# Kernel tuning notes

Hardware: AMD Instinct MI355X
Metric: run time of the kernel (lower is better)

## Reference

```python
import jax, jax.numpy as jnp
import numpy as np

EMBED_DIM = 512
NUM_HEADS = 8
WINDOW = 64
FFN_RATIO = 4


def _mha(q_in, kv_in, w_in, b_in, w_out, b_out, n_heads, mask=None):
    # Faithful torch.nn.MultiheadAttention (batch_first) with packed in_proj.
    b, sq, d = q_in.shape
    sk = kv_in.shape[1]
    hd = d // n_heads
    wq, wk, wv = jnp.split(w_in, 3, axis=0)   # each [d, d]
    bq, bk, bv = jnp.split(b_in, 3, axis=0)
    q = (q_in @ wq.T + bq).reshape(b, sq, n_heads, hd).transpose(0, 2, 1, 3)
    k = (kv_in @ wk.T + bk).reshape(b, sk, n_heads, hd).transpose(0, 2, 1, 3)
    v = (kv_in @ wv.T + bv).reshape(b, sk, n_heads, hd).transpose(0, 2, 1, 3)
    scores = jnp.einsum('bhqd,bhkd->bhqk', q, k) / jnp.sqrt(jnp.asarray(hd, q.dtype))
    if mask is not None:
        scores = scores + mask  # additive -inf mask, broadcast over [b, h]
    attn = jax.nn.softmax(scores, axis=-1)
    out = jnp.einsum('bhqk,bhkd->bhqd', attn, v)
    out = out.transpose(0, 2, 1, 3).reshape(b, sq, d)
    return out @ w_out.T + b_out


def _layernorm(x, g, b, eps=1e-5):
    mu = jnp.mean(x, axis=-1, keepdims=True)
    var = jnp.var(x, axis=-1, keepdims=True)
    return (x - mu) * jax.lax.rsqrt(var + eps) * g + b


def _local_causal_mask(p, window, dtype=jnp.float32):
    # row i attends to columns [max(0, i-window), i]
    i = jnp.arange(p)[:, None]
    j = jnp.arange(p)[None, :]
    allowed = (j <= i) & (j >= i - window)
    return jnp.where(allowed, jnp.zeros((), dtype), jnp.asarray(-jnp.inf, dtype))


def setup_inputs() -> dict:
    key = jax.random.key(0)
    ks = jax.random.split(key, 20)
    d, h = EMBED_DIM, EMBED_DIM * FFN_RATIO
    s = 0.02
    return {
        'x': jax.random.normal(ks[0], (64, 512, d), jnp.float32),
        'anchors': jax.random.normal(ks[1], (64, 32, d), jnp.float32),
        'lw_in': jax.random.normal(ks[2], (3 * d, d), jnp.float32) * s,
        'lb_in': jnp.zeros((3 * d,), jnp.float32),
        'lw_out': jax.random.normal(ks[3], (d, d), jnp.float32) * s,
        'lb_out': jnp.zeros((d,), jnp.float32),
        'gw_in': jax.random.normal(ks[4], (3 * d, d), jnp.float32) * s,
        'gb_in': jnp.zeros((3 * d,), jnp.float32),
        'gw_out': jax.random.normal(ks[5], (d, d), jnp.float32) * s,
        'gb_out': jnp.zeros((d,), jnp.float32),
        'w1': jax.random.normal(ks[6], (h, d), jnp.float32) * s,
        'b1': jnp.zeros((h,), jnp.float32),
        'w2': jax.random.normal(ks[7], (d, h), jnp.float32) * s,
        'b2': jnp.zeros((d,), jnp.float32),
        'g1': jnp.ones((d,), jnp.float32),
        'be1': jnp.zeros((d,), jnp.float32),
        'g2': jnp.ones((d,), jnp.float32),
        'be2': jnp.zeros((d,), jnp.float32),
    }


def reference(x, anchors, lw_in, lb_in, lw_out, lb_out, gw_in, gb_in, gw_out, gb_out,
              w1, b1, w2, b2, g1, be1, g2, be2):
    p = x.shape[1]
    mask = _local_causal_mask(p, WINDOW, x.dtype)
    x = x + _mha(x, x, lw_in, lb_in, lw_out, lb_out, NUM_HEADS, mask)
    x = x + _mha(x, anchors, gw_in, gb_in, gw_out, gb_out, NUM_HEADS)
    x = _layernorm(x, g1, be1)
    h = jax.nn.gelu(x @ w1.T + b1, approximate=False)
    ffn = h @ w2.T + b2
    return _layernorm(x + ffn, g2, be2)
```

## Files before the change

kernel.cpp:

```cpp
#include <hip/hip_runtime.h>
#include <cmath>


typedef unsigned short u16;
typedef unsigned int u32;
typedef __bf16 bf16_t;
typedef bf16_t bf16x8 __attribute__((ext_vector_type(8)));
typedef float f32x4 __attribute__((ext_vector_type(4)));

#define DEV __device__ __forceinline__

DEV u16 f2b(float f) {
  u32 u = __float_as_uint(f);
  u32 r = u + 0x7fffu + ((u >> 16) & 1u);
  return (u16)(r >> 16);
}
DEV float b2f(u16 b) { return __uint_as_float(((u32)b) << 16); }

DEV void g2l16(const void* g, void* l) {
  __builtin_amdgcn_global_load_lds((const __attribute__((address_space(1))) void*)g,
                                   (__attribute__((address_space(3))) void*)l,
                                   16, 0, 0);
}

__global__ __launch_bounds__(256) void conv1(const float* __restrict__ s,
                                             u16* __restrict__ d) {
  size_t idx = ((size_t)blockIdx.x * 256 + threadIdx.x) * 8;
  float4 a = *(const float4*)(s + idx);
  float4 b = *(const float4*)(s + idx + 4);
  float v[8] = {a.x, a.y, a.z, a.w, b.x, b.y, b.z, b.w};
  union { u16 q[8]; uint4 u; } pk;
#pragma unroll
  for (int i = 0; i < 8; ++i) pk.q[i] = f2b(v[i]);
  *(uint4*)(d + idx) = pk.u;
}

template <bool GELU, bool RES32, bool RESB, bool OUT32, bool OUTB>
__global__ __launch_bounds__(256) void gemm_bt(
    const u16* __restrict__ A, const u16* __restrict__ B,
    const float* __restrict__ bias, const float* __restrict__ res32,
    const u16* __restrict__ resb, float* __restrict__ out32,
    u16* __restrict__ outb, int M, int N, int K) {
  __shared__ __align__(16) char smem[17408];
  u16* lA = (u16*)smem;
  u16* lB = (u16*)(smem + 8192);
  const int tid = threadIdx.x;
  const int lane = tid & 63, wv = tid >> 6;
  const int m0 = blockIdx.y * 128, n0 = blockIdx.x * 128;
  const int wm = (wv >> 1) * 64, wn = (wv & 1) * 64;
  const int lrow = lane & 15;
  const int quad = lane >> 4;
  const int koff = quad * 8;
  const int rA = tid >> 2;
  const int cA = (tid & 3) * 8;

  f32x4 zero4 = {0.f, 0.f, 0.f, 0.f};
  f32x4 acc[4][4];
#pragma unroll
  for (int a = 0; a < 4; ++a)
#pragma unroll
    for (int b = 0; b < 4; ++b) acc[a][b] = zero4;

  for (int kt = 0; kt < K; kt += 32) {
    const u16* gA = A + (size_t)m0 * K + kt;
    const u16* gB = B + (size_t)n0 * K + kt;
#pragma unroll
    for (int it = 0; it < 2; ++it) {
      int row = it * 64 + rA;
      int c = it * 256 + tid;
      g2l16(gA + (size_t)row * K + cA, (char*)lA + (size_t)c * 16);
      g2l16(gB + (size_t)row * K + cA, (char*)lB + (size_t)c * 16);
    }
    __syncthreads();
    bf16x8 af[4], bfr[4];
#pragma unroll
    for (int f = 0; f < 4; ++f)
      af[f] = *(const bf16x8*)&lA[(wm + f * 16 + lrow) * 32 + koff];
#pragma unroll
    for (int f = 0; f < 4; ++f)
      bfr[f] = *(const bf16x8*)&lB[(wn + f * 16 + lrow) * 32 + koff];
#pragma unroll
    for (int fm = 0; fm < 4; ++fm)
#pragma unroll
      for (int fn = 0; fn < 4; ++fn)
        acc[fm][fn] = __builtin_amdgcn_mfma_f32_16x16x32_bf16(af[fm], bfr[fn], acc[fm][fn], 0, 0, 0);
    __syncthreads();
  }
  float* cw = (float*)(smem + (size_t)wv * 4352);

  const int row16 = lane >> 2;
  const int c0 = (lane & 3) * 16;
  const int gcb = n0 + wn + c0;
  float bias16[16];
#pragma unroll
  for (int t = 0; t < 4; ++t) {
    float4 b4 = *(const float4*)(bias + gcb + t * 4);
    bias16[t * 4 + 0] = b4.x; bias16[t * 4 + 1] = b4.y;
    bias16[t * 4 + 2] = b4.z; bias16[t * 4 + 3] = b4.w;
  }

#pragma unroll
  for (int fm = 0; fm < 4; ++fm) {
#pragma unroll
    for (int fn = 0; fn < 4; ++fn)
#pragma unroll
      for (int r = 0; r < 4; ++r)
        cw[(quad * 4 + r) * 68 + fn * 16 + lrow] = acc[fm][fn][r];
    const int grow = m0 + wm + fm * 16 + row16;
    const size_t gbase = (size_t)grow * N + gcb;
    const float* crp = &cw[row16 * 68 + c0];
    float v[16];
#pragma unroll
    for (int t = 0; t < 4; ++t) {
      f32x4 q = *(const f32x4*)(crp + t * 4);
      v[t * 4 + 0] = q[0] + bias16[t * 4 + 0];
      v[t * 4 + 1] = q[1] + bias16[t * 4 + 1];
      v[t * 4 + 2] = q[2] + bias16[t * 4 + 2];
      v[t * 4 + 3] = q[3] + bias16[t * 4 + 3];
    }
    if (RES32) {
#pragma unroll
      for (int t = 0; t < 4; ++t) {
        float4 rr = *(const float4*)(res32 + gbase + t * 4);
        v[t * 4 + 0] += rr.x; v[t * 4 + 1] += rr.y;
        v[t * 4 + 2] += rr.z; v[t * 4 + 3] += rr.w;
      }
    }
    if (RESB) {
#pragma unroll
      for (int t = 0; t < 2; ++t) {
        union { u16 q[8]; uint4 u; } rb;
        rb.u = *(const uint4*)(resb + gbase + t * 8);
#pragma unroll
        for (int j = 0; j < 8; ++j) v[t * 8 + j] += b2f(rb.q[j]);
      }
    }
    if (GELU) {
#pragma unroll
      for (int e = 0; e < 16; ++e)
        v[e] = 0.5f * v[e] * (1.0f + erff(v[e] * 0.70710678118654752f));
    }
    if (OUT32) {
#pragma unroll
      for (int t = 0; t < 4; ++t) {
        float4 w4 = {v[t * 4 + 0], v[t * 4 + 1], v[t * 4 + 2], v[t * 4 + 3]};
        *(float4*)(out32 + gbase + t * 4) = w4;
      }
    }
    if (OUTB) {
#pragma unroll
      for (int t = 0; t < 2; ++t) {
        union { u16 q[8]; uint4 u; } pk;
#pragma unroll
        for (int j = 0; j < 8; ++j) pk.q[j] = f2b(v[t * 8 + j]);
        *(uint4*)(outb + gbase + t * 8) = pk.u;
      }
    }
  }
}

__global__ __launch_bounds__(256) void local_attn_mfma(const u16* __restrict__ qkv,
                                                       u16* __restrict__ outb) {
  __shared__ u16 vt[64][152];
  __shared__ u16 pb[4][16][104];
  const int tid = threadIdx.x;
  const int lane = tid & 63, w = tid >> 6;
  const int c = lane & 15, quad = lane >> 4;
  const int bx = blockIdx.x;
  const int qb = bx & 7, h = (bx >> 3) & 7, bb = bx >> 6;
  const int i0 = qb * 64;
  const int hc = h * 64;
  const size_t rbase = (size_t)bb * 512;

  {
    int r = tid >> 1;
    int d0 = (tid & 1) * 32;
    int key = i0 - 64 + r;
    if (key < 0) key = 0;
    if (key > 511) key = 511;
    const u16* Vr = qkv + (rbase + key) * 1536 + 1024 + hc + d0;
#pragma unroll
    for (int g = 0; g < 4; ++g) {
      union { u16 q[8]; uint4 u; } vv;
      vv.u = *(const uint4*)(Vr + g * 8);
#pragma unroll
      for (int j = 0; j < 8; ++j) vt[d0 + g * 8 + j][r] = vv.q[j];
    }
    if (tid < 128) {
      int r2 = 128 + (tid >> 3);
      int d2 = (tid & 7) * 8;
      int key2 = i0 - 64 + r2;
      if (key2 < 0) key2 = 0;
      if (key2 > 511) key2 = 511;
      const u16* Vr2 = qkv + (rbase + key2) * 1536 + 1024 + hc + d2;
      union { u16 q[8]; uint4 u; } vv2;
      vv2.u = *(const uint4*)Vr2;
#pragma unroll
      for (int j = 0; j < 8; ++j) vt[d2 + j][r2] = vv2.q[j];
    }
  }
  __syncthreads();

  const int i0w = i0 + 16 * w;
  const int kg0 = i0w - 64;

  bf16x8 qf0, qf1;
  {
    const u16* Qr = qkv + (rbase + i0w + c) * 1536 + hc + quad * 8;
    qf0 = *(const bf16x8*)Qr;
    qf1 = *(const bf16x8*)(Qr + 32);
  }

  f32x4 s[5];
#pragma unroll
  for (int kb = 0; kb < 5; ++kb) {
    int key = kg0 + kb * 16 + c; if (key < 0) key = 0;
    const u16* Kr = qkv + (rbase + key) * 1536 + 512 + hc + quad * 8;
    bf16x8 k0 = *(const bf16x8*)Kr;
    bf16x8 k1 = *(const bf16x8*)(Kr + 32);
    f32x4 z = {0.f, 0.f, 0.f, 0.f};
    z = __builtin_amdgcn_mfma_f32_16x16x32_bf16(qf0, k0, z, 0, 0, 0);
    s[kb] = __builtin_amdgcn_mfma_f32_16x16x32_bf16(qf1, k1, z, 0, 0, 0);
  }

  float mx[4];
#pragma unroll
  for (int r = 0; r < 4; ++r) {
    int row = quad * 4 + r;
    float m = -1e30f;
#pragma unroll
    for (int kb = 0; kb < 5; ++kb) {
      float v = s[kb][r] * 0.125f;
      int key = kg0 + kb * 16 + c;
      bool ok = key >= 0;
      if (kb == 0) ok = ok && (c >= row);
      if (kb == 4) ok = ok && (c <= row);
      v = ok ? v : -1e30f;
      s[kb][r] = v;
      m = fmaxf(m, v);
    }
    mx[r] = m;
  }
#pragma unroll
  for (int o = 1; o <= 8; o <<= 1)
#pragma unroll
    for (int r = 0; r < 4; ++r) mx[r] = fmaxf(mx[r], __shfl_xor(mx[r], o));

  float l[4] = {0.f, 0.f, 0.f, 0.f};
#pragma unroll
  for (int kb = 0; kb < 5; ++kb)
#pragma unroll
    for (int r = 0; r < 4; ++r) {
      u16 pq = f2b(__expf(s[kb][r] - mx[r]));
      l[r] += b2f(pq);
      pb[w][quad * 4 + r][kb * 16 + c] = pq;
    }
#pragma unroll
  for (int r = 0; r < 4; ++r) pb[w][quad * 4 + r][80 + c] = 0;
#pragma unroll
  for (int o = 1; o <= 8; o <<= 1)
#pragma unroll
    for (int r = 0; r < 4; ++r) l[r] += __shfl_xor(l[r], o);
  float inv[4];
#pragma unroll
  for (int r = 0; r < 4; ++r) inv[r] = 1.f / l[r];

  f32x4 o4[4];
#pragma unroll
  for (int nb = 0; nb < 4; ++nb) o4[nb] = f32x4{0.f, 0.f, 0.f, 0.f};
#pragma unroll
  for (int kt = 0; kt < 3; ++kt) {
    bf16x8 pa = *(const bf16x8*)&pb[w][c][kt * 32 + quad * 8];
#pragma unroll
    for (int nb = 0; nb < 4; ++nb) {
      bf16x8 vb = *(const bf16x8*)&vt[nb * 16 + c][16 * w + kt * 32 + quad * 8];
      o4[nb] = __builtin_amdgcn_mfma_f32_16x16x32_bf16(pa, vb, o4[nb], 0, 0, 0);
    }
  }
#pragma unroll
  for (int nb = 0; nb < 4; ++nb)
#pragma unroll
    for (int r = 0; r < 4; ++r) {
      int seq = i0w + quad * 4 + r;
      outb[(rbase + seq) * 512 + hc + nb * 16 + c] = f2b(o4[nb][r] * inv[r]);
    }
}

__global__ __launch_bounds__(256) void global_attn_mfma(const u16* __restrict__ qg,
                                                        const u16* __restrict__ kvg,
                                                        u16* __restrict__ outb) {
  __shared__ u16 vt[64][40];
  __shared__ u16 pb[4][16][40];
  const int tid = threadIdx.x;
  const int lane = tid & 63, w = tid >> 6;
  const int c = lane & 15, quad = lane >> 4;
  const int bx = blockIdx.x;
  const int qb = bx & 7, h = (bx >> 3) & 7, bb = bx >> 6;
  const int i0 = qb * 64;
  const int hc = h * 64;
  const size_t rbase = (size_t)bb * 512;

  {
    int r = tid >> 3;
    int d0 = (tid & 7) * 8;
    const u16* Vr = kvg + ((size_t)bb * 32 + r) * 1024 + 512 + hc + d0;
    union { u16 q[8]; uint4 u; } vv;
    vv.u = *(const uint4*)Vr;
#pragma unroll
    for (int j = 0; j < 8; ++j) vt[d0 + j][r] = vv.q[j];
  }
  __syncthreads();

  const int i0w = i0 + 16 * w;
  bf16x8 qf0, qf1;
  {
    const u16* Qr = qg + (rbase + i0w + c) * 512 + hc + quad * 8;
    qf0 = *(const bf16x8*)Qr;
    qf1 = *(const bf16x8*)(Qr + 32);
  }
  f32x4 s[2];
#pragma unroll
  for (int kb = 0; kb < 2; ++kb) {
    const u16* Kr = kvg + ((size_t)bb * 32 + kb * 16 + c) * 1024 + hc + quad * 8;
    bf16x8 k0 = *(const bf16x8*)Kr;
    bf16x8 k1 = *(const bf16x8*)(Kr + 32);
    f32x4 z = {0.f, 0.f, 0.f, 0.f};
    z = __builtin_amdgcn_mfma_f32_16x16x32_bf16(qf0, k0, z, 0, 0, 0);
    s[kb] = __builtin_amdgcn_mfma_f32_16x16x32_bf16(qf1, k1, z, 0, 0, 0);
  }
  float mx[4];
#pragma unroll
  for (int r = 0; r < 4; ++r)
    mx[r] = fmaxf(s[0][r] * 0.125f, s[1][r] * 0.125f);
#pragma unroll
  for (int o = 1; o <= 8; o <<= 1)
#pragma unroll
    for (int r = 0; r < 4; ++r) mx[r] = fmaxf(mx[r], __shfl_xor(mx[r], o));
  float l[4] = {0.f, 0.f, 0.f, 0.f};
#pragma unroll
  for (int kb = 0; kb < 2; ++kb)
#pragma unroll
    for (int r = 0; r < 4; ++r) {
      u16 pq = f2b(__expf(s[kb][r] * 0.125f - mx[r]));
      l[r] += b2f(pq);
      pb[w][quad * 4 + r][kb * 16 + c] = pq;
    }
#pragma unroll
  for (int o = 1; o <= 8; o <<= 1)
#pragma unroll
    for (int r = 0; r < 4; ++r) l[r] += __shfl_xor(l[r], o);
  float inv[4];
#pragma unroll
  for (int r = 0; r < 4; ++r) inv[r] = 1.f / l[r];

  f32x4 o4[4];
#pragma unroll
  for (int nb = 0; nb < 4; ++nb) o4[nb] = f32x4{0.f, 0.f, 0.f, 0.f};
  bf16x8 pa = *(const bf16x8*)&pb[w][c][quad * 8];
#pragma unroll
  for (int nb = 0; nb < 4; ++nb) {
    bf16x8 vb = *(const bf16x8*)&vt[nb * 16 + c][quad * 8];
    o4[nb] = __builtin_amdgcn_mfma_f32_16x16x32_bf16(pa, vb, o4[nb], 0, 0, 0);
  }
#pragma unroll
  for (int nb = 0; nb < 4; ++nb)
#pragma unroll
    for (int r = 0; r < 4; ++r) {
      int seq = i0w + quad * 4 + r;
      outb[(rbase + seq) * 512 + hc + nb * 16 + c] = f2b(o4[nb][r] * inv[r]);
    }
}

__global__ __launch_bounds__(256) void ln_b2b(const u16* __restrict__ in,
                                              const float* __restrict__ gg,
                                              const float* __restrict__ bb,
                                              u16* __restrict__ outb) {
  const int lane = threadIdx.x & 63;
  const size_t row = (size_t)blockIdx.x * 4 + (threadIdx.x >> 6);
  union { u16 q[8]; uint4 u; } pk;
  pk.u = *(const uint4*)(in + row * 512 + lane * 8);
  float v[8];
#pragma unroll
  for (int e = 0; e < 8; ++e) v[e] = b2f(pk.q[e]);
  float sm = 0.f, sq = 0.f;
#pragma unroll
  for (int e = 0; e < 8; ++e) { sm += v[e]; sq += v[e] * v[e]; }
#pragma unroll
  for (int o = 32; o; o >>= 1) { sm += __shfl_xor(sm, o); sq += __shfl_xor(sq, o); }
  float mean = sm * (1.0f / 512.0f);
  float var = sq * (1.0f / 512.0f) - mean * mean;
  float rs = rsqrtf(var + 1e-5f);
  float4 ga = *(const float4*)(gg + lane * 8);
  float4 gb = *(const float4*)(gg + lane * 8 + 4);
  float4 ba = *(const float4*)(bb + lane * 8);
  float4 bbv = *(const float4*)(bb + lane * 8 + 4);
  float gv[8] = {ga.x, ga.y, ga.z, ga.w, gb.x, gb.y, gb.z, gb.w};
  float bv[8] = {ba.x, ba.y, ba.z, ba.w, bbv.x, bbv.y, bbv.z, bbv.w};
  union { u16 q[8]; uint4 u; } po;
#pragma unroll
  for (int e = 0; e < 8; ++e) po.q[e] = f2b((v[e] - mean) * rs * gv[e] + bv[e]);
  *(uint4*)(outb + row * 512 + lane * 8) = po.u;
}

__global__ __launch_bounds__(256) void ln_f2f(const float* __restrict__ in,
                                              const float* __restrict__ gg,
                                              const float* __restrict__ bb,
                                              float* __restrict__ out) {
  const int lane = threadIdx.x & 63;
  const size_t row = (size_t)blockIdx.x * 4 + (threadIdx.x >> 6);
  const float* p = in + row * 512 + lane * 8;
  float4 a = *(const float4*)p;
  float4 b = *(const float4*)(p + 4);
  float v[8] = {a.x, a.y, a.z, a.w, b.x, b.y, b.z, b.w};
  float sm = 0.f, sq = 0.f;
#pragma unroll
  for (int e = 0; e < 8; ++e) { sm += v[e]; sq += v[e] * v[e]; }
#pragma unroll
  for (int o = 32; o; o >>= 1) { sm += __shfl_xor(sm, o); sq += __shfl_xor(sq, o); }
  float mean = sm * (1.0f / 512.0f);
  float var = sq * (1.0f / 512.0f) - mean * mean;
  float rs = rsqrtf(var + 1e-5f);
  float4 ga = *(const float4*)(gg + lane * 8);
  float4 gb = *(const float4*)(gg + lane * 8 + 4);
  float4 ba = *(const float4*)(bb + lane * 8);
  float4 bbv = *(const float4*)(bb + lane * 8 + 4);
  float gv[8] = {ga.x, ga.y, ga.z, ga.w, gb.x, gb.y, gb.z, gb.w};
  float bv[8] = {ba.x, ba.y, ba.z, ba.w, bbv.x, bbv.y, bbv.z, bbv.w};
  float r[8];
#pragma unroll
  for (int e = 0; e < 8; ++e) r[e] = (v[e] - mean) * rs * gv[e] + bv[e];
  float4 r1 = {r[0], r[1], r[2], r[3]};
  float4 r2 = {r[4], r[5], r[6], r[7]};
  *(float4*)(out + row * 512 + lane * 8) = r1;
  *(float4*)(out + row * 512 + lane * 8 + 4) = r2;
}

extern "C" void kernel_launch(void* const* d_in, const int* in_sizes, int n_in,
                              void* d_out, int out_size, void* d_ws, size_t ws_size,
                              hipStream_t stream) {
  const float* x      = (const float*)d_in[0];
  const float* anchors= (const float*)d_in[1];
  const float* lw_in  = (const float*)d_in[2];
  const float* lb_in  = (const float*)d_in[3];
  const float* lw_out = (const float*)d_in[4];
  const float* lb_out = (const float*)d_in[5];
  const float* gw_in  = (const float*)d_in[6];
  const float* gb_in  = (const float*)d_in[7];
  const float* gw_out = (const float*)d_in[8];
  const float* gb_out = (const float*)d_in[9];
  const float* w1     = (const float*)d_in[10];
  const float* b1     = (const float*)d_in[11];
  const float* w2     = (const float*)d_in[12];
  const float* b2     = (const float*)d_in[13];
  const float* g1     = (const float*)d_in[14];
  const float* be1    = (const float*)d_in[15];
  const float* g2     = (const float*)d_in[16];
  const float* be2    = (const float*)d_in[17];
  (void)in_sizes; (void)n_in; (void)out_size;
  float* out = (float*)d_out;

  char* ws = (char*)d_ws;
  size_t o = 0;
  auto nxt = [&](size_t bytes) { char* p = ws + o; o += bytes; return p; };
  u16* lwib = (u16*)nxt((size_t)1536 * 512 * 2);
  u16* lwob = (u16*)nxt((size_t)512 * 512 * 2);
  u16* gwib = (u16*)nxt((size_t)1536 * 512 * 2);
  u16* gwob = (u16*)nxt((size_t)512 * 512 * 2);
  u16* w1b  = (u16*)nxt((size_t)2048 * 512 * 2);
  u16* w2b  = (u16*)nxt((size_t)512 * 2048 * 2);
  u16* ab   = (u16*)nxt((size_t)2048 * 512 * 2);
  u16* kvgb = (u16*)nxt((size_t)2048 * 1024 * 2);
  const size_t wbytes = o;

  int nc = 1;
  while (wbytes + (size_t)(32768 / nc) * 6144 > ws_size && nc < 32) nc <<= 1;
  const int Mc = 32768 / nc;
  const int nBat = Mc / 512;
  u16* BIGb = (u16*)nxt((size_t)Mc * 4096);
  u16* Pb   = (u16*)nxt((size_t)Mc * 1024);
  u16* Qb   = (u16*)nxt((size_t)Mc * 1024);
  u16* Sb   = BIGb + (size_t)Mc * 1536;

  conv1<<<384, 256, 0, stream>>>(lw_in, lwib);
  conv1<<<128, 256, 0, stream>>>(lw_out, lwob);
  conv1<<<384, 256, 0, stream>>>(gw_in, gwib);
  conv1<<<128, 256, 0, stream>>>(gw_out, gwob);
  conv1<<<512, 256, 0, stream>>>(w1, w1b);
  conv1<<<512, 256, 0, stream>>>(w2, w2b);
  conv1<<<512, 256, 0, stream>>>(anchors, ab);
  gemm_bt<false, false, false, false, true><<<dim3(8, 16), 256, 0, stream>>>(
      ab, gwib + 512 * 512, gb_in + 512, nullptr, nullptr, nullptr, kvgb, 2048, 1024, 512);

  for (int ck = 0; ck < nc; ++ck) {
    const size_t r0 = (size_t)ck * Mc;
    const float* xck = x + r0 * 512;
    conv1<<<Mc / 4, 256, 0, stream>>>(xck, Pb);
    gemm_bt<false, false, false, false, true><<<dim3(12, Mc / 128), 256, 0, stream>>>(
        Pb, lwib, lb_in, nullptr, nullptr, nullptr, BIGb, Mc, 1536, 512);
    local_attn_mfma<<<nBat * 64, 256, 0, stream>>>(BIGb, Sb);
    gemm_bt<false, true, false, false, true><<<dim3(4, Mc / 128), 256, 0, stream>>>(
        Sb, lwob, lb_out, xck, nullptr, nullptr, Qb, Mc, 512, 512);
    gemm_bt<false, false, false, false, true><<<dim3(4, Mc / 128), 256, 0, stream>>>(
        Qb, gwib, gb_in, nullptr, nullptr, nullptr, Pb, Mc, 512, 512);
    global_attn_mfma<<<nBat * 64, 256, 0, stream>>>(Pb, kvgb + (r0 / 512) * 32 * 1024, Sb);
    gemm_bt<false, false, true, false, true><<<dim3(4, Mc / 128), 256, 0, stream>>>(
        Sb, gwob, gb_out, nullptr, Qb, nullptr, Pb, Mc, 512, 512);
    ln_b2b<<<Mc / 4, 256, 0, stream>>>(Pb, g1, be1, Qb);
    gemm_bt<true, false, false, false, true><<<dim3(16, Mc / 128), 256, 0, stream>>>(
        Qb, w1b, b1, nullptr, nullptr, nullptr, BIGb, Mc, 2048, 512);
    gemm_bt<false, false, true, true, false><<<dim3(4, Mc / 128), 256, 0, stream>>>(
        BIGb, w2b, b2, nullptr, Qb, out + r0 * 512, nullptr, Mc, 512, 2048);
    ln_f2f<<<Mc / 4, 256, 0, stream>>>(out + r0 * 512, g2, be2, out + r0 * 512);
  }
}
```

Baseline: 731.4 us.

## Replace 128x128 GEMM with pipelined 256x256 swizzled-LDS MFMA kernel

Replaces the simple 128x128, K=32 tile GEMM with a 256x256 tile, 512-thread kernel. It streams K in 64-wide steps through double-buffered, XOR-swizzled LDS, interleaving global-to-LDS prefetches with MFMA phases under raised wave priority. It also remaps block indices across XCDs for locality. The aim is more data reuse per tile and hiding load latency behind compute. The cost is 128KB of LDS per block and fewer blocks on the narrow-N GEMMs.

```diff
diff --git a/kernel.cpp b/kernel.cpp
--- a/kernel.cpp
+++ b/kernel.cpp
@@ -9,6 +9,7 @@
 typedef float f32x4 __attribute__((ext_vector_type(4)));
 
 #define DEV __device__ __forceinline__
+#define MFMA16(a, b, c) __builtin_amdgcn_mfma_f32_16x16x32_bf16(a, b, c, 0, 0, 0)
 
 DEV u16 f2b(float f) {
   u32 u = __float_as_uint(f);
@@ -36,61 +37,154 @@
 }
 
 template <bool GELU, bool RES32, bool RESB, bool OUT32, bool OUTB>
-__global__ __launch_bounds__(256) void gemm_bt(
+__global__ __launch_bounds__(512, 2) void gemm256(
     const u16* __restrict__ A, const u16* __restrict__ B,
     const float* __restrict__ bias, const float* __restrict__ res32,
     const u16* __restrict__ resb, float* __restrict__ out32,
     u16* __restrict__ outb, int M, int N, int K) {
-  __shared__ __align__(16) char smem[17408];
-  u16* lA = (u16*)smem;
-  u16* lB = (u16*)(smem + 8192);
+  __shared__ __align__(16) char smem[131072];
   const int tid = threadIdx.x;
   const int lane = tid & 63, wv = tid >> 6;
-  const int m0 = blockIdx.y * 128, n0 = blockIdx.x * 128;
-  const int wm = (wv >> 1) * 64, wn = (wv & 1) * 64;
-  const int lrow = lane & 15;
-  const int quad = lane >> 4;
-  const int koff = quad * 8;
-  const int rA = tid >> 2;
-  const int cA = (tid & 3) * 8;
-
+  const int warp_m = wv >> 2, warp_n = wv & 3;
+  const int lrow = lane & 15, quad = lane >> 4;
+
+  int idx = blockIdx.x;
+  {
+    const int nwg = gridDim.x;
+    if (nwg >= 8) {
+      const int q = nwg >> 3, r = nwg & 7;
+      const int xcd = idx & 7, rk = idx >> 3;
+      idx = (xcd < r ? xcd * (q + 1) : r * (q + 1) + (xcd - r) * q) + rk;
+    }
+  }
+  const int nx = N >> 8;
+  const int m0 = (idx / nx) * 256, n0 = (idx % nx) * 256;
+
+  const int srow = wv * 8 + (lane >> 3);
+  const int scol = (((lane & 7) ^ ((lane >> 3) & 7)) << 4);
+  const int sdst = wv * 1024 + lane * 16;
+  const int x4 = (lane & 7) << 4;
+  const int col0 = (quad * 16) ^ x4;
+  const int col1 = (64 + quad * 16) ^ x4;
+  const int aRowB = lrow * 128;
+  const int bRowB = ((warp_n & 1) * 64 + lrow) * 128;
+
+  const int nt = K >> 6;
+
+  auto stageH = [&](const u16* __restrict__ G, int row0, int kt, int ldsOff) {
+    const char* g0 = (const char*)G + (((size_t)(row0 + srow) * K + kt * 64) << 1) + scol;
+    char* l0 = smem + ldsOff + sdst;
+    g2l16(g0, l0);
+    g2l16(g0 + ((size_t)K << 7), l0 + 8192);
+  };
+
+  f32x4 acc[8][4];
   f32x4 zero4 = {0.f, 0.f, 0.f, 0.f};
-  f32x4 acc[4][4];
-#pragma unroll
-  for (int a = 0; a < 4; ++a)
+#pragma unroll
+  for (int a = 0; a < 8; ++a)
 #pragma unroll
     for (int b = 0; b < 4; ++b) acc[a][b] = zero4;
 
-  for (int kt = 0; kt < K; kt += 32) {
-    const u16* gA = A + (size_t)m0 * K + kt;
-    const u16* gB = B + (size_t)n0 * K + kt;
-#pragma unroll
-    for (int it = 0; it < 2; ++it) {
-      int row = it * 64 + rA;
-      int c = it * 256 + tid;
-      g2l16(gA + (size_t)row * K + cA, (char*)lA + (size_t)c * 16);
-      g2l16(gB + (size_t)row * K + cA, (char*)lB + (size_t)c * 16);
-    }
-    __syncthreads();
-    bf16x8 af[4], bfr[4];
-#pragma unroll
-    for (int f = 0; f < 4; ++f)
-      af[f] = *(const bf16x8*)&lA[(wm + f * 16 + lrow) * 32 + koff];
-#pragma unroll
-    for (int f = 0; f < 4; ++f)
-      bfr[f] = *(const bf16x8*)&lB[(wn + f * 16 + lrow) * 32 + koff];
-#pragma unroll
-    for (int fm = 0; fm < 4; ++fm)
-#pragma unroll
-      for (int fn = 0; fn < 4; ++fn)
-        acc[fm][fn] = __builtin_amdgcn_mfma_f32_16x16x32_bf16(af[fm], bfr[fn], acc[fm][fn], 0, 0, 0);
-    __syncthreads();
-  }
+  stageH(A, m0, 0, 0);
+  stageH(A, m0 + 128, 0, 16384);
+  stageH(B, n0, 0, 65536);
+  stageH(B, n0 + 128, 0, 65536 + 16384);
+  stageH(A, m0, 1, 32768);
+  stageH(A, m0 + 128, 1, 32768 + 16384);
+  asm volatile("s_waitcnt vmcnt(4)" ::: "memory");
+  asm volatile("s_barrier" ::: "memory");
+
+  int cur = 0;
+  bf16x8 afr[8][2], bfr[2][2];
+  for (int kt = 0; kt < nt; ++kt) {
+    const char* cA = smem + cur * 32768 + warp_m * 16384;
+    const char* cB = smem + 65536 + cur * 32768 + (warp_n >> 1) * 16384;
+    const int nb = cur ^ 1;
+    const int kt1 = (kt + 1 < nt) ? kt + 1 : nt - 1;
+    const int kt2 = (kt + 2 < nt) ? kt + 2 : nt - 1;
+
+#pragma unroll
+    for (int m = 0; m < 4; ++m) {
+      afr[m][0] = *(const bf16x8*)(cA + aRowB + m * 2048 + col0);
+      afr[m][1] = *(const bf16x8*)(cA + aRowB + m * 2048 + col1);
+    }
+#pragma unroll
+    for (int n = 0; n < 2; ++n) {
+      bfr[n][0] = *(const bf16x8*)(cB + bRowB + n * 2048 + col0);
+      bfr[n][1] = *(const bf16x8*)(cB + bRowB + n * 2048 + col1);
+    }
+    stageH(B, n0, kt1, 65536 + nb * 32768);
+    asm volatile("s_barrier" ::: "memory");
+    __builtin_amdgcn_s_setprio(1);
+#pragma unroll
+    for (int m = 0; m < 4; ++m)
+#pragma unroll
+      for (int n = 0; n < 2; ++n) {
+        acc[m][n] = MFMA16(afr[m][0], bfr[n][0], acc[m][n]);
+        acc[m][n] = MFMA16(afr[m][1], bfr[n][1], acc[m][n]);
+      }
+    __builtin_amdgcn_s_setprio(0);
+    asm volatile("s_barrier" ::: "memory");
+
+#pragma unroll
+    for (int m = 4; m < 8; ++m) {
+      afr[m][0] = *(const bf16x8*)(cA + aRowB + m * 2048 + col0);
+      afr[m][1] = *(const bf16x8*)(cA + aRowB + m * 2048 + col1);
+    }
+    stageH(B, n0 + 128, kt1, 65536 + nb * 32768 + 16384);
+    asm volatile("s_barrier" ::: "memory");
+    __builtin_amdgcn_s_setprio(1);
+#pragma unroll
+    for (int m = 4; m < 8; ++m)
+#pragma unroll
+      for (int n = 0; n < 2; ++n) {
+        acc[m][n] = MFMA16(afr[m][0], bfr[n][0], acc[m][n]);
+        acc[m][n] = MFMA16(afr[m][1], bfr[n][1], acc[m][n]);
+      }
+    __builtin_amdgcn_s_setprio(0);
+    asm volatile("s_barrier" ::: "memory");
+
+#pragma unroll
+    for (int n = 0; n < 2; ++n) {
+      bfr[n][0] = *(const bf16x8*)(cB + bRowB + (n + 2) * 2048 + col0);
+      bfr[n][1] = *(const bf16x8*)(cB + bRowB + (n + 2) * 2048 + col1);
+    }
+    stageH(A, m0, kt2, cur * 32768);
+    asm volatile("s_barrier" ::: "memory");
+    __builtin_amdgcn_s_setprio(1);
+#pragma unroll
+    for (int m = 0; m < 4; ++m)
+#pragma unroll
+      for (int n = 0; n < 2; ++n) {
+        acc[m][n + 2] = MFMA16(afr[m][0], bfr[n][0], acc[m][n + 2]);
+        acc[m][n + 2] = MFMA16(afr[m][1], bfr[n][1], acc[m][n + 2]);
+      }
+    __builtin_amdgcn_s_setprio(0);
+    asm volatile("s_barrier" ::: "memory");
+
+    stageH(A, m0 + 128, kt2, cur * 32768 + 16384);
+    asm volatile("s_barrier" ::: "memory");
+    __builtin_amdgcn_s_setprio(1);
+#pragma unroll
+    for (int m = 4; m < 8; ++m)
+#pragma unroll
+      for (int n = 0; n < 2; ++n) {
+        acc[m][n + 2] = MFMA16(afr[m][0], bfr[n][0], acc[m][n + 2]);
+        acc[m][n + 2] = MFMA16(afr[m][1], bfr[n][1], acc[m][n + 2]);
+      }
+    __builtin_amdgcn_s_setprio(0);
+    asm volatile("s_waitcnt vmcnt(4)" ::: "memory");
+    asm volatile("s_barrier" ::: "memory");
+    cur = nb;
+  }
+
+  asm volatile("s_waitcnt vmcnt(0)" ::: "memory");
+  __syncthreads();
+
   float* cw = (float*)(smem + (size_t)wv * 4352);
-
   const int row16 = lane >> 2;
   const int c0 = (lane & 3) * 16;
-  const int gcb = n0 + wn + c0;
+  const int gcb = n0 + warp_n * 64 + c0;
   float bias16[16];
 #pragma unroll
   for (int t = 0; t < 4; ++t) {
@@ -100,13 +194,13 @@
   }
 
 #pragma unroll
-  for (int fm = 0; fm < 4; ++fm) {
+  for (int fm = 0; fm < 8; ++fm) {
 #pragma unroll
     for (int fn = 0; fn < 4; ++fn)
 #pragma unroll
       for (int r = 0; r < 4; ++r)
         cw[(quad * 4 + r) * 68 + fn * 16 + lrow] = acc[fm][fn][r];
-    const int grow = m0 + wm + fm * 16 + row16;
+    const int grow = m0 + warp_m * 128 + fm * 16 + row16;
     const size_t gbase = (size_t)grow * N + gcb;
     const float* crp = &cw[row16 * 68 + c0];
     float v[16];
@@ -476,6 +570,7 @@
   while (wbytes + (size_t)(32768 / nc) * 6144 > ws_size && nc < 32) nc <<= 1;
   const int Mc = 32768 / nc;
   const int nBat = Mc / 512;
+  const int mb = Mc >> 8;
   u16* BIGb = (u16*)nxt((size_t)Mc * 4096);
   u16* Pb   = (u16*)nxt((size_t)Mc * 1024);
   u16* Qb   = (u16*)nxt((size_t)Mc * 1024);
@@ -488,27 +583,27 @@
   conv1<<<512, 256, 0, stream>>>(w1, w1b);
   conv1<<<512, 256, 0, stream>>>(w2, w2b);
   conv1<<<512, 256, 0, stream>>>(anchors, ab);
-  gemm_bt<false, false, false, false, true><<<dim3(8, 16), 256, 0, stream>>>(
+  gemm256<false, false, false, false, true><<<8 * 4, 512, 0, stream>>>(
       ab, gwib + 512 * 512, gb_in + 512, nullptr, nullptr, nullptr, kvgb, 2048, 1024, 512);
 
   for (int ck = 0; ck < nc; ++ck) {
     const size_t r0 = (size_t)ck * Mc;
     const float* xck = x + r0 * 512;
     conv1<<<Mc / 4, 256, 0, stream>>>(xck, Pb);
-    gemm_bt<false, false, false, false, true><<<dim3(12, Mc / 128), 256, 0, stream>>>(
+    gemm256<false, false, false, false, true><<<mb * 6, 512, 0, stream>>>(
         Pb, lwib, lb_in, nullptr, nullptr, nullptr, BIGb, Mc, 1536, 512);
     local_attn_mfma<<<nBat * 64, 256, 0, stream>>>(BIGb, Sb);
-    gemm_bt<false, true, false, false, true><<<dim3(4, Mc / 128), 256, 0, stream>>>(
+    gemm256<false, true, false, false, true><<<mb * 2, 512, 0, stream>>>(
         Sb, lwob, lb_out, xck, nullptr, nullptr, Qb, Mc, 512, 512);
-    gemm_bt<false, false, false, false, true><<<dim3(4, Mc / 128), 256, 0, stream>>>(
+    gemm256<false, false, false, false, true><<<mb * 2, 512, 0, stream>>>(
         Qb, gwib, gb_in, nullptr, nullptr, nullptr, Pb, Mc, 512, 512);
     global_attn_mfma<<<nBat * 64, 256, 0, stream>>>(Pb, kvgb + (r0 / 512) * 32 * 1024, Sb);
-    gemm_bt<false, false, true, false, true><<<dim3(4, Mc / 128), 256, 0, stream>>>(
+    gemm256<false, false, true, false, true><<<mb * 2, 512, 0, stream>>>(
         Sb, gwob, gb_out, nullptr, Qb, nullptr, Pb, Mc, 512, 512);
     ln_b2b<<<Mc / 4, 256, 0, stream>>>(Pb, g1, be1, Qb);
-    gemm_bt<true, false, false, false, true><<<dim3(16, Mc / 128), 256, 0, stream>>>(
+    gemm256<true, false, false, false, true><<<mb * 8, 512, 0, stream>>>(
         Qb, w1b, b1, nullptr, nullptr, nullptr, BIGb, Mc, 2048, 512);
-    gemm_bt<false, false, true, true, false><<<dim3(4, Mc / 128), 256, 0, stream>>>(
+    gemm256<false, false, true, true, false><<<mb * 2, 512, 0, stream>>>(
         BIGb, w2b, b2, nullptr, Qb, out + r0 * 512, nullptr, Mc, 512, 2048);
     ln_f2f<<<Mc / 4, 256, 0, stream>>>(out + r0 * 512, g2, be2, out + r0 * 512);
   }
```

Result: faster. 640.6 us (-12.4%).

## Rewrite GEMM with 128x256 tiles, triple-buffered LDS pipeline, XCD swizzle, fast GELU

Applied to the files above, without the earlier changes.

Replaces the single-buffered 128x128 GEMM with a 512-thread kernel that computes 128x256 tiles. It uses a three-slot LDS ring with global_load_lds prefetch two k-steps ahead, manual waitcnt/barrier scheduling, XOR-swizzled LDS addressing and a remap of block indices across XCDs. The exact erff in the GELU epilogue is replaced by an Abramowitz-Stegun polynomial approximation. The goal is to hide global load latency behind MFMA and reduce LDS bank conflicts, at the cost of more LDS per block and a small GELU approximation error.

```diff
diff --git a/kernel.cpp b/kernel.cpp
--- a/kernel.cpp
+++ b/kernel.cpp
@@ -9,6 +9,8 @@
 typedef float f32x4 __attribute__((ext_vector_type(4)));
 
 #define DEV __device__ __forceinline__
+#define MFMA16(a, b, c) __builtin_amdgcn_mfma_f32_16x16x32_bf16(a, b, c, 0, 0, 0)
+#define SBAR() __builtin_amdgcn_sched_barrier(0)
 
 DEV u16 f2b(float f) {
   u32 u = __float_as_uint(f);
@@ -16,6 +18,19 @@
   return (u16)(r >> 16);
 }
 DEV float b2f(u16 b) { return __uint_as_float(((u32)b) << 16); }
+
+DEV float gelu_erf(float x) {
+  float y = x * 0.70710678118654752f;
+  float ay = fabsf(y);
+  float t = __builtin_amdgcn_rcpf(1.0f + 0.3275911f * ay);
+  float p = t * (0.254829592f +
+            t * (-0.284496736f +
+            t * (1.421413741f +
+            t * (-1.453152027f + t * 1.061405429f))));
+  float e = 1.0f - p * __expf(-y * y);
+  float erfv = (y < 0.f) ? -e : e;
+  return 0.5f * x * (1.0f + erfv);
+}
 
 DEV void g2l16(const void* g, void* l) {
   __builtin_amdgcn_global_load_lds((const __attribute__((address_space(1))) void*)g,
@@ -36,61 +51,98 @@
 }
 
 template <bool GELU, bool RES32, bool RESB, bool OUT32, bool OUTB>
-__global__ __launch_bounds__(256) void gemm_bt(
+__global__ __launch_bounds__(512, 4) void gemm128(
     const u16* __restrict__ A, const u16* __restrict__ B,
     const float* __restrict__ bias, const float* __restrict__ res32,
     const u16* __restrict__ resb, float* __restrict__ out32,
     u16* __restrict__ outb, int M, int N, int K) {
-  __shared__ __align__(16) char smem[17408];
-  u16* lA = (u16*)smem;
-  u16* lB = (u16*)(smem + 8192);
+  __shared__ __align__(16) char smem[73728];
   const int tid = threadIdx.x;
   const int lane = tid & 63, wv = tid >> 6;
-  const int m0 = blockIdx.y * 128, n0 = blockIdx.x * 128;
-  const int wm = (wv >> 1) * 64, wn = (wv & 1) * 64;
-  const int lrow = lane & 15;
-  const int quad = lane >> 4;
-  const int koff = quad * 8;
-  const int rA = tid >> 2;
-  const int cA = (tid & 3) * 8;
-
+  const int warp_m = wv >> 2, warp_n = wv & 3;
+  const int lrow = lane & 15, quad = lane >> 4;
+
+  int idx = blockIdx.x;
+  {
+    const int nwg = gridDim.x;
+    if (nwg >= 8) {
+      const int q = nwg >> 3, r = nwg & 7;
+      const int xcd = idx & 7, rk = idx >> 3;
+      idx = (xcd < r ? xcd * (q + 1) : r * (q + 1) + (xcd - r) * q) + rk;
+    }
+  }
+  const int nx = N >> 8;
+  const int m0 = (idx / nx) * 128, n0 = (idx % nx) * 256;
+
+  const int srow = tid >> 2;
+  const int scol = (((tid & 3) ^ ((tid >> 3) & 3)) << 4);
+  const int sdst = tid * 16;
+  const int cs = (quad * 16) ^ (((lrow >> 1) & 3) << 4);
+  const int rdA = warp_m * 4096 + lrow * 64 + cs;
+  const int rdB = warp_n * 4096 + lrow * 64 + cs;
+
+  const int nt = K >> 5;
+
+  auto stage3 = [&](int kt, int slot) {
+    const char* ga = (const char*)A + (((size_t)(m0 + srow) * K + kt * 32) << 1) + scol;
+    g2l16(ga, smem + slot * 8192 + sdst);
+    const char* gb = (const char*)B + (((size_t)(n0 + srow) * K + kt * 32) << 1) + scol;
+    char* lb = smem + 24576 + slot * 16384 + sdst;
+    g2l16(gb, lb);
+    g2l16(gb + ((size_t)K << 8), lb + 8192);
+  };
+
+  f32x4 acc[4][4];
   f32x4 zero4 = {0.f, 0.f, 0.f, 0.f};
-  f32x4 acc[4][4];
 #pragma unroll
   for (int a = 0; a < 4; ++a)
 #pragma unroll
     for (int b = 0; b < 4; ++b) acc[a][b] = zero4;
 
-  for (int kt = 0; kt < K; kt += 32) {
-    const u16* gA = A + (size_t)m0 * K + kt;
-    const u16* gB = B + (size_t)n0 * K + kt;
-#pragma unroll
-    for (int it = 0; it < 2; ++it) {
-      int row = it * 64 + rA;
-      int c = it * 256 + tid;
-      g2l16(gA + (size_t)row * K + cA, (char*)lA + (size_t)c * 16);
-      g2l16(gB + (size_t)row * K + cA, (char*)lB + (size_t)c * 16);
-    }
-    __syncthreads();
-    bf16x8 af[4], bfr[4];
-#pragma unroll
-    for (int f = 0; f < 4; ++f)
-      af[f] = *(const bf16x8*)&lA[(wm + f * 16 + lrow) * 32 + koff];
-#pragma unroll
-    for (int f = 0; f < 4; ++f)
-      bfr[f] = *(const bf16x8*)&lB[(wn + f * 16 + lrow) * 32 + koff];
-#pragma unroll
-    for (int fm = 0; fm < 4; ++fm)
-#pragma unroll
-      for (int fn = 0; fn < 4; ++fn)
-        acc[fm][fn] = __builtin_amdgcn_mfma_f32_16x16x32_bf16(af[fm], bfr[fn], acc[fm][fn], 0, 0, 0);
-    __syncthreads();
-  }
+  stage3(0, 0);
+  stage3(1, 1);
+  SBAR();
+  asm volatile("s_waitcnt vmcnt(3)" ::: "memory");
+  asm volatile("s_barrier" ::: "memory");
+  SBAR();
+
+  int c0s = 0, c2s = 2;
+  for (int kt = 0; kt < nt; ++kt) {
+    const char* cA = smem + c0s * 8192;
+    const char* cB = smem + 24576 + c0s * 16384;
+    bf16x8 afr[4], bfr[4];
+#pragma unroll
+    for (int m = 0; m < 4; ++m) afr[m] = *(const bf16x8*)(cA + rdA + m * 1024);
+#pragma unroll
+    for (int n = 0; n < 4; ++n) bfr[n] = *(const bf16x8*)(cB + rdB + n * 1024);
+    const int kt2 = (kt + 2 < nt) ? kt + 2 : nt - 1;
+    stage3(kt2, c2s);
+    SBAR();
+    asm volatile("s_barrier" ::: "memory");
+    asm volatile("s_waitcnt lgkmcnt(0)" ::: "memory");
+    SBAR();
+    __builtin_amdgcn_s_setprio(1);
+#pragma unroll
+    for (int m = 0; m < 4; ++m)
+#pragma unroll
+      for (int n = 0; n < 4; ++n)
+        acc[m][n] = MFMA16(afr[m], bfr[n], acc[m][n]);
+    __builtin_amdgcn_s_setprio(0);
+    SBAR();
+    asm volatile("s_waitcnt vmcnt(3)" ::: "memory");
+    asm volatile("s_barrier" ::: "memory");
+    SBAR();
+    c0s = (c0s == 2) ? 0 : c0s + 1;
+    c2s = (c2s == 2) ? 0 : c2s + 1;
+  }
+
+  asm volatile("s_waitcnt vmcnt(0)" ::: "memory");
+  __syncthreads();
+
   float* cw = (float*)(smem + (size_t)wv * 4352);
-
   const int row16 = lane >> 2;
   const int c0 = (lane & 3) * 16;
-  const int gcb = n0 + wn + c0;
+  const int gcb = n0 + warp_n * 64 + c0;
   float bias16[16];
 #pragma unroll
   for (int t = 0; t < 4; ++t) {
@@ -106,7 +158,7 @@
 #pragma unroll
       for (int r = 0; r < 4; ++r)
         cw[(quad * 4 + r) * 68 + fn * 16 + lrow] = acc[fm][fn][r];
-    const int grow = m0 + wm + fm * 16 + row16;
+    const int grow = m0 + warp_m * 64 + fm * 16 + row16;
     const size_t gbase = (size_t)grow * N + gcb;
     const float* crp = &cw[row16 * 68 + c0];
     float v[16];
@@ -137,8 +189,7 @@
     }
     if (GELU) {
 #pragma unroll
-      for (int e = 0; e < 16; ++e)
-        v[e] = 0.5f * v[e] * (1.0f + erff(v[e] * 0.70710678118654752f));
+      for (int e = 0; e < 16; ++e) v[e] = gelu_erf(v[e]);
     }
     if (OUT32) {
 #pragma unroll
@@ -476,6 +527,7 @@
   while (wbytes + (size_t)(32768 / nc) * 6144 > ws_size && nc < 32) nc <<= 1;
   const int Mc = 32768 / nc;
   const int nBat = Mc / 512;
+  const int mb7 = Mc >> 7;
   u16* BIGb = (u16*)nxt((size_t)Mc * 4096);
   u16* Pb   = (u16*)nxt((size_t)Mc * 1024);
   u16* Qb   = (u16*)nxt((size_t)Mc * 1024);
@@ -488,27 +540,27 @@
   conv1<<<512, 256, 0, stream>>>(w1, w1b);
   conv1<<<512, 256, 0, stream>>>(w2, w2b);
   conv1<<<512, 256, 0, stream>>>(anchors, ab);
-  gemm_bt<false, false, false, false, true><<<dim3(8, 16), 256, 0, stream>>>(
+  gemm128<false, false, false, false, true><<<16 * 4, 512, 0, stream>>>(
       ab, gwib + 512 * 512, gb_in + 512, nullptr, nullptr, nullptr, kvgb, 2048, 1024, 512);
 
   for (int ck = 0; ck < nc; ++ck) {
     const size_t r0 = (size_t)ck * Mc;
     const float* xck = x + r0 * 512;
     conv1<<<Mc / 4, 256, 0, stream>>>(xck, Pb);
-    gemm_bt<false, false, false, false, true><<<dim3(12, Mc / 128), 256, 0, stream>>>(
+    gemm128<false, false, false, false, true><<<mb7 * 6, 512, 0, stream>>>(
         Pb, lwib, lb_in, nullptr, nullptr, nullptr, BIGb, Mc, 1536, 512);
     local_attn_mfma<<<nBat * 64, 256, 0, stream>>>(BIGb, Sb);
-    gemm_bt<false, true, false, false, true><<<dim3(4, Mc / 128), 256, 0, stream>>>(
+    gemm128<false, true, false, false, true><<<mb7 * 2, 512, 0, stream>>>(
         Sb, lwob, lb_out, xck, nullptr, nullptr, Qb, Mc, 512, 512);
-    gemm_bt<false, false, false, false, true><<<dim3(4, Mc / 128), 256, 0, stream>>>(
+    gemm128<false, false, false, false, true><<<mb7 * 2, 512, 0, stream>>>(
         Qb, gwib, gb_in, nullptr, nullptr, nullptr, Pb, Mc, 512, 512);
     global_attn_mfma<<<nBat * 64, 256, 0, stream>>>(Pb, kvgb + (r0 / 512) * 32 * 1024, Sb);
-    gemm_bt<false, false, true, false, true><<<dim3(4, Mc / 128), 256, 0, stream>>>(
+    gemm128<false, false, true, false, true><<<mb7 * 2, 512, 0, stream>>>(
         Sb, gwob, gb_out, nullptr, Qb, nullptr, Pb, Mc, 512, 512);
     ln_b2b<<<Mc / 4, 256, 0, stream>>>(Pb, g1, be1, Qb);
-    gemm_bt<true, false, false, false, true><<<dim3(16, Mc / 128), 256, 0, stream>>>(
+    gemm128<true, false, false, false, true><<<mb7 * 8, 512, 0, stream>>>(
         Qb, w1b, b1, nullptr, nullptr, nullptr, BIGb, Mc, 2048, 512);
-    gemm_bt<false, false, true, true, false><<<dim3(4, Mc / 128), 256, 0, stream>>>(
+    gemm128<false, false, true, true, false><<<mb7 * 2, 512, 0, stream>>>(
         BIGb, w2b, b2, nullptr, Qb, out + r0 * 512, nullptr, Mc, 512, 2048);
     ln_f2f<<<Mc / 4, 256, 0, stream>>>(out + r0 * 512, g2, be2, out + r0 * 512);
   }
```

Measured after the change: 629.0 us. 1.16x faster.
